# Performance work log

Hardware: AMD Instinct MI355X
Metric: run time of the kernel (lower is better)

The kernel has to match this reference:

```python
import jax, jax.numpy as jnp
import numpy as np

N, K, E = 100000, 256, 3200000
IN_C, H1, H2 = 5, 16, 32


def _glorot(key, shape):
    fan = shape[0]
    return jax.random.normal(key, shape, jnp.float32) / np.float32(np.sqrt(fan))


def setup_inputs() -> dict:
    key = jax.random.key(0)
    ks = jax.random.split(key, 14)
    x = jax.random.normal(ks[0], (N, IN_C), jnp.float32)
    edge_index = jax.random.randint(ks[1], (2, E), 0, N, dtype=jnp.int64)
    edge_attr = jax.random.uniform(ks[2], (E,), jnp.float32)
    pos = jax.random.uniform(ks[3], (N, K), jnp.float32)  # soft cluster assignment s_c
    return {
        "x": x, "edge_index": edge_index, "edge_attr": edge_attr, "pos": pos,
        # SplineConv1 (kernel_size=1 -> single kernel weight + root + bias)
        "W1": _glorot(ks[4], (IN_C, H1)), "root1": _glorot(ks[5], (IN_C, H1)),
        "b1": jnp.zeros((H1,), jnp.float32),
        # SplineConv2
        "W2": _glorot(ks[6], (H1, H2)), "root2": _glorot(ks[7], (H1, H2)),
        "b2": jnp.zeros((H2,), jnp.float32),
        # MLP head
        "lw1": _glorot(ks[8], (H2, 8)), "lb1": jnp.zeros((8,), jnp.float32),
        "lw2": _glorot(ks[9], (8, 2)), "lb2": jnp.zeros((2,), jnp.float32),
    }


def _leaky(v):
    return jnp.where(v > 0, v, 0.1 * v)


def reference(x, edge_index, edge_attr, pos, W1, root1, b1, W2, root2, b2, lw1, lb1, lw2, lb2):
    n = x.shape[0]
    src, dst = edge_index[0], edge_index[1]  # source_to_target flow

    # --- SplineConv(5,16,dim=1,kernel_size=1): mean_j (x_j @ W) + x @ root + b ---
    msg = x[src] @ W1                                      # [E,16]
    agg = jax.ops.segment_sum(msg, dst, num_segments=n)    # [N,16]
    deg = jax.ops.segment_sum(jnp.ones((msg.shape[0],), x.dtype), dst, num_segments=n)
    h = agg / jnp.maximum(deg, 1.0)[:, None] + x @ root1 + b1
    h = _leaky(jax.nn.relu(h))                             # relu then LeakyReLU(0.1)

    # --- pooling: x' = s_c^T h ; adj = s_c^T A s_c (A sparse with edge_attr values) ---
    xp = pos.T @ h                                          # [K,16]
    A_sc = jax.ops.segment_sum(edge_attr[:, None] * pos[dst], src, num_segments=n)  # spmm: [N,K]
    adj = pos.T @ A_sc                                      # [K,K]

    # --- nonzero/coalesce -> edge list of adj; SplineConv(16,32) on pooled graph ---
    # kernel_size=1 => edge values irrelevant; only the nonzero pattern (connectivity) matters.
    mask = (adj != 0).astype(x.dtype)                       # [K,K], row=src, col=dst
    xw = xp @ W2                                            # [K,32]
    deg2 = mask.sum(axis=0)                                 # in-degree per target
    agg2 = (mask.T @ xw) / jnp.maximum(deg2, 1.0)[:, None]
    h2 = agg2 + xp @ root2 + b2
    h2 = _leaky(jax.nn.relu(h2))                            # [K,32]

    # --- global mean pool (single graph) + MLP head, return x[0] ---
    g = h2.mean(axis=0)                                     # [32]
    out = _leaky(g @ lw1 + lb1) @ lw2 + lb2                 # [2]
    return out
```

## Files before the change

### kernel.cpp

```cpp
#include <hip/hip_runtime.h>

#define INC 5
#define H1C 16
#define H2C 32
#define KCL 256

#define NBINS 40
#define BINSZ 2500
#define MAXCHUNK 12

#define PB_SHIFT 9
#define PB_SZ 512
#define PB_NBMAX 256
#define PB_C 18432
#define PB_M 6144
#define PB_ETPB 6
#define PB_S 2
#define PB_GMAX 9216
#define PB_GETG 9

#define POOL_NB 512
#define PT 32

typedef __attribute__((address_space(1))) const unsigned gls_src;
typedef __attribute__((address_space(3))) unsigned gls_dst;

__global__ void k_setup(const float* __restrict__ x, float* __restrict__ x8,
                        const unsigned int* __restrict__ ei, int* __restrict__ flag,
                        unsigned* __restrict__ gcur, int N, int NB) {
    int n = blockIdx.x * blockDim.x + threadIdx.x;
    if (n < N) {
        const float* xr = x + (size_t)n * INC;
        float4* o = (float4*)(x8 + (size_t)n * 8);
        o[0] = make_float4(xr[0], xr[1], xr[2], xr[3]);
        o[1] = make_float4(xr[4], 0.0f, 0.0f, 0.0f);
    }
    if (blockIdx.x == 0) {
        if (threadIdx.x < (unsigned)NB) gcur[threadIdx.x] = (unsigned)threadIdx.x * PB_C;
        if (threadIdx.x == 0) {
            int is64 = 1;
            for (int i = 1; i < 32; i += 2)
                if (ei[i] != 0u) is64 = 0;
            *flag = is64;
        }
    }
}

__global__ void k_detect(const unsigned int* __restrict__ ei, int* __restrict__ flag) {
    if (blockIdx.x == 0 && threadIdx.x == 0) {
        int is64 = 1;
        for (int i = 1; i < 32; i += 2)
            if (ei[i] != 0u) is64 = 0;
        *flag = is64;
    }
}

__global__ __launch_bounds__(1024) void k_part(const unsigned int* __restrict__ ei,
                                               const int* __restrict__ flag,
                                               unsigned* __restrict__ gcur,
                                               unsigned* __restrict__ bucket,
                                               int E, int NB) {
    __shared__ int hist[PB_NBMAX];
    __shared__ int lbase[PB_NBMAX];
    __shared__ unsigned gbase[PB_NBMAX];
    __shared__ int sc[PB_NBMAX];
    __shared__ unsigned sorted[PB_M];
    __shared__ unsigned char sbin[PB_M];

    const int tid = threadIdx.x;
    const int e0 = blockIdx.x * PB_M;
    int m = E - e0; if (m > PB_M) m = PB_M;

    for (int i = tid; i < PB_NBMAX; i += 1024) hist[i] = 0;
    __syncthreads();

    const int is64 = *flag;
    unsigned ee[PB_ETPB]; int eb[PB_ETPB]; int er[PB_ETPB];

#pragma unroll
    for (int ii = 0; ii < PB_ETPB; ii++) {
        const int off = tid + ii * 1024;
        eb[ii] = -1; ee[ii] = 0u; er[ii] = 0;
        if (off < m) {
            const int e = e0 + off;
            unsigned d, s;
            if (is64) { d = ei[2 * ((size_t)E + (size_t)e)]; s = ei[2 * (size_t)e]; }
            else      { d = ei[(size_t)E + (size_t)e];       s = ei[(size_t)e]; }
            const int b = (int)(d >> PB_SHIFT);
            eb[ii] = b;
            ee[ii] = (s << PB_SHIFT) | (d & (PB_SZ - 1));
            er[ii] = atomicAdd(&hist[b], 1);
        }
    }
    __syncthreads();

    if (tid < PB_NBMAX) sc[tid] = hist[tid];
    __syncthreads();
    for (int st = 1; st < PB_NBMAX; st <<= 1) {
        int v = 0;
        if (tid < PB_NBMAX && tid >= st) v = sc[tid - st];
        __syncthreads();
        if (tid < PB_NBMAX) sc[tid] += v;
        __syncthreads();
    }
    if (tid < PB_NBMAX) lbase[tid] = sc[tid] - hist[tid];
    if (tid < NB) gbase[tid] = atomicAdd(&gcur[tid], (unsigned)hist[tid]);
    __syncthreads();

#pragma unroll
    for (int ii = 0; ii < PB_ETPB; ii++) {
        if (eb[ii] >= 0) {
            const int j = lbase[eb[ii]] + er[ii];
            sorted[j] = ee[ii];
            sbin[j] = (unsigned char)eb[ii];
        }
    }
    __syncthreads();

    for (int j = tid; j < m; j += 1024) {
        const int b = (int)sbin[j];
        const unsigned g = gbase[b] + (unsigned)(j - lbase[b]);
        if (g < (unsigned)(b + 1) * PB_C) bucket[g] = sorted[j];
    }
}

__global__ __launch_bounds__(1024) void k_gather(const unsigned* __restrict__ bucket,
                                                 const unsigned* __restrict__ gcur,
                                                 const float* __restrict__ x8,
                                                 float* __restrict__ part,
                                                 int N, int NB) {
    __shared__ unsigned sorted[PB_GMAX];
    __shared__ int hist[PB_SZ];
    __shared__ int sc[PB_SZ];
    __shared__ int lbase[PB_SZ];
    __shared__ float stage[PB_SZ * 6];

    const int b = blockIdx.x / PB_S;
    const int sub = blockIdx.x % PB_S;
    const int tid = threadIdx.x;
    const int lo = b << PB_SHIFT;
    int hi = lo + PB_SZ; if (hi > N) hi = N;
    const int nloc = hi - lo;

    int cnt = (int)(gcur[b] - (unsigned)b * PB_C);
    if (cnt > PB_C) cnt = PB_C;
    const int i0 = (cnt * sub) / PB_S;
    const int i1 = (cnt * (sub + 1)) / PB_S;
    const int m = i1 - i0;
    const unsigned* bk = bucket + (size_t)b * PB_C + i0;

    for (int i = tid; i < PB_SZ; i += 1024) hist[i] = 0;
    __syncthreads();

    unsigned ee[PB_GETG]; int edl[PB_GETG]; int er[PB_GETG];
#pragma unroll
    for (int ii = 0; ii < PB_GETG; ii++) {
        const int off = tid + ii * 1024;
        edl[ii] = -1; ee[ii] = 0u; er[ii] = 0;
        if (off < m) {
            const unsigned e = bk[off];
            const int dl = (int)(e & (PB_SZ - 1));
            edl[ii] = dl;
            ee[ii] = e;
            er[ii] = atomicAdd(&hist[dl], 1);
        }
    }
    __syncthreads();

    if (tid < PB_SZ) sc[tid] = hist[tid];
    __syncthreads();
    for (int st = 1; st < PB_SZ; st <<= 1) {
        int v = 0;
        if (tid < PB_SZ && tid >= st) v = sc[tid - st];
        __syncthreads();
        if (tid < PB_SZ) sc[tid] += v;
        __syncthreads();
    }
    if (tid < PB_SZ) lbase[tid] = sc[tid] - hist[tid];
    __syncthreads();

#pragma unroll
    for (int ii = 0; ii < PB_GETG; ii++)
        if (edl[ii] >= 0) sorted[lbase[edl[ii]] + er[ii]] = ee[ii];
    __syncthreads();

    const int node = tid & (PB_SZ - 1);
    const int half = tid >> PB_SHIFT;
    const int start = lbase[node];
    const int len = hist[node];
    const int js = start + (half ? (len >> 1) : 0);
    const int je = start + (half ? len : (len >> 1));
    float a0 = 0.f, a1 = 0.f, a2 = 0.f, a3 = 0.f, a4 = 0.f;
    for (int j = js; j < je; j++) {
        const unsigned s = sorted[j] >> PB_SHIFT;
        const float4 xr4 = *(const float4*)(x8 + (size_t)s * 8);
        const float xr5 = x8[(size_t)s * 8 + 4];
        a0 += xr4.x; a1 += xr4.y; a2 += xr4.z; a3 += xr4.w; a4 += xr5;
    }
    if (half) {
        float* st = stage + node * 6;
        st[0] = a0; st[1] = a1; st[2] = a2; st[3] = a3; st[4] = a4;
    }
    __syncthreads();
    if (!half && node < nloc) {
        const float* st = stage + node * 6;
        float* o = part + (size_t)sub * ((size_t)N * 6) + (size_t)(lo + node) * 6;
        o[0] = a0 + st[0];
        o[1] = a1 + st[1];
        o[2] = a2 + st[2];
        o[3] = a3 + st[3];
        o[4] = a4 + st[4];
        o[5] = (float)len;
    }
}

__global__ __launch_bounds__(1024) void k_edge_bin(const unsigned int* __restrict__ ei,
                                                   const float* __restrict__ x,
                                                   const int* __restrict__ flag,
                                                   float* __restrict__ part,
                                                   int E, int nchunk, int N) {
    __shared__ float acc[BINSZ * 6];
    const int bin = blockIdx.x % NBINS;
    const int chunk = blockIdx.x / NBINS;
    const int lo = bin * BINSZ;
    const int hi = (lo + BINSZ < N) ? (lo + BINSZ) : N;
    const int nloc = hi - lo;
    for (int i = threadIdx.x; i < nloc * 6; i += 1024) acc[i] = 0.0f;
    __syncthreads();

    const int is64 = *flag;
    const long long ce = ((long long)E + nchunk - 1) / nchunk;
    const long long e0 = (long long)chunk * ce;
    long long e1 = e0 + ce;
    if (e1 > E) e1 = E;

    for (long long e = e0 + threadIdx.x; e < e1; e += 1024) {
        const int d = is64 ? (int)ei[2 * ((size_t)E + (size_t)e)] : (int)ei[(size_t)E + (size_t)e];
        if (d >= lo && d < hi) {
            const int s = is64 ? (int)ei[2 * (size_t)e] : (int)ei[(size_t)e];
            const float* xr = x + (size_t)s * INC;
            float* a = acc + (d - lo) * 6;
            atomicAdd(a + 0, xr[0]);
            atomicAdd(a + 1, xr[1]);
            atomicAdd(a + 2, xr[2]);
            atomicAdd(a + 3, xr[3]);
            atomicAdd(a + 4, xr[4]);
            atomicAdd(a + 5, 1.0f);
        }
    }
    __syncthreads();
    float* o = part + (size_t)chunk * ((size_t)N * 6) + (size_t)lo * 6;
    for (int i = threadIdx.x; i < nloc * 6; i += 1024) o[i] = acc[i];
}

__global__ void k_node2(const float* __restrict__ x, const float* __restrict__ part,
                        const float* __restrict__ W1, const float* __restrict__ root1,
                        const float* __restrict__ b1, float* __restrict__ h,
                        int N, int nchunk) {
    int n = blockIdx.x * blockDim.x + threadIdx.x;
    if (n >= N) return;
    float s[6] = {0.f, 0.f, 0.f, 0.f, 0.f, 0.f};
    for (int c = 0; c < nchunk; c++) {
        const float* p = part + (size_t)c * ((size_t)N * 6) + (size_t)n * 6;
#pragma unroll
        for (int j = 0; j < 6; j++) s[j] += p[j];
    }
    const float inv = 1.0f / fmaxf(s[5], 1.0f);
    float xs[INC], xv[INC];
#pragma unroll
    for (int c = 0; c < INC; c++) {
        xs[c] = s[c] * inv;
        xv[c] = x[(size_t)n * INC + c];
    }
    float hv[H1C];
#pragma unroll
    for (int j = 0; j < H1C; j++) {
        float v = b1[j];
#pragma unroll
        for (int c = 0; c < INC; c++)
            v = fmaf(xs[c], W1[c * H1C + j], fmaf(xv[c], root1[c * H1C + j], v));
        hv[j] = fmaxf(v, 0.0f);
    }
    float4* hp = (float4*)(h + (size_t)n * H1C);
#pragma unroll
    for (int q = 0; q < 4; q++)
        hp[q] = make_float4(hv[4 * q], hv[4 * q + 1], hv[4 * q + 2], hv[4 * q + 3]);
}

__global__ __launch_bounds__(512) void k_pool(const float* __restrict__ pos,
                                              const float* __restrict__ h,
                                              float* __restrict__ xp_part, int N, int nb) {
    __shared__ float pbuf[2][PT * KCL];
    __shared__ float hbuf[2][PT * H1C];
    const int tid = threadIdx.x;
    const int k = tid & 255;
    const int jh = tid >> 8;
    const int wid = tid >> 6;
    const int lane = tid & 63;
    const int chunk = (N + nb - 1) / nb;
    const int n0 = blockIdx.x * chunk;
    const int n1 = min(n0 + chunk, N);
    const int ntile = (n1 > n0) ? (n1 - n0 + PT - 1) / PT : 0;

    const size_t maxp = (size_t)N * KCL - 4;
    const size_t maxh = (size_t)N * H1C - 4;

    float acc[8];
#pragma unroll
    for (int j = 0; j < 8; j++) acc[j] = 0.0f;

    auto STAGE = [&](int bf, int tile) {
        const size_t nt0 = (size_t)n0 + (size_t)tile * PT;
        const size_t pb = nt0 * KCL;
#pragma unroll
        for (int c = 0; c < 4; ++c) {
            const int off = (wid * 4 + c) * 256;
            size_t fi = pb + (size_t)off + (size_t)lane * 4;
            if (fi > maxp) fi = maxp;
            __builtin_amdgcn_global_load_lds((gls_src*)(pos + fi),
                                             (gls_dst*)&pbuf[bf][off], 16, 0, 0);
        }
        if (wid < 2) {
            const int off = wid * 256;
            size_t fi = nt0 * H1C + (size_t)off + (size_t)lane * 4;
            if (fi > maxh) fi = maxh;
            __builtin_amdgcn_global_load_lds((gls_src*)(h + fi),
                                             (gls_dst*)&hbuf[bf][off], 16, 0, 0);
        }
    };

    int buf = 0;
    if (ntile > 0) {
        STAGE(0, 0);
        __syncthreads();
    }
    for (int t = 0; t < ntile; ++t) {
        if (t + 1 < ntile) STAGE(buf ^ 1, t + 1);
        const int nt0 = n0 + t * PT;
        const int tcnt = min(PT, n1 - nt0);
        for (int tt = 0; tt < tcnt; ++tt) {
            const float p = pbuf[buf][tt * KCL + k];
            const float4* hr = (const float4*)&hbuf[buf][tt * H1C + jh * 8];
            const float4 ha = hr[0], hb = hr[1];
            acc[0] = fmaf(p, ha.x, acc[0]); acc[1] = fmaf(p, ha.y, acc[1]);
            acc[2] = fmaf(p, ha.z, acc[2]); acc[3] = fmaf(p, ha.w, acc[3]);
            acc[4] = fmaf(p, hb.x, acc[4]); acc[5] = fmaf(p, hb.y, acc[5]);
            acc[6] = fmaf(p, hb.z, acc[6]); acc[7] = fmaf(p, hb.w, acc[7]);
        }
        __syncthreads();
        buf ^= 1;
    }

    float* o = xp_part + (size_t)blockIdx.x * (KCL * H1C) + k * H1C + jh * 8;
    *(float4*)o = make_float4(acc[0], acc[1], acc[2], acc[3]);
    *(float4*)(o + 4) = make_float4(acc[4], acc[5], acc[6], acc[7]);
}

__global__ __launch_bounds__(1024) void k_xpred(const float* __restrict__ xp_part,
                                                float* __restrict__ xp, int nb) {
    __shared__ float r[1024];
    const int li = threadIdx.x & 63;
    const int sub = threadIdx.x >> 6;
    const int i = blockIdx.x * 64 + li;
    float s = 0.0f;
    for (int b = sub; b < nb; b += 16) s += xp_part[(size_t)b * (KCL * H1C) + i];
    r[threadIdx.x] = s;
    __syncthreads();
    if (threadIdx.x < 512) r[threadIdx.x] += r[threadIdx.x + 512];
    __syncthreads();
    if (threadIdx.x < 256) r[threadIdx.x] += r[threadIdx.x + 256];
    __syncthreads();
    if (threadIdx.x < 128) r[threadIdx.x] += r[threadIdx.x + 128];
    __syncthreads();
    if (threadIdx.x < 64) xp[i] = r[threadIdx.x] + r[threadIdx.x + 64];
}

__global__ __launch_bounds__(256) void k_tail(const float* __restrict__ xp,
                                              const float* __restrict__ W2,
                                              const float* __restrict__ root2,
                                              const float* __restrict__ b2,
                                              const float* __restrict__ lw1,
                                              const float* __restrict__ lb1,
                                              const float* __restrict__ lw2,
                                              const float* __restrict__ lb2,
                                              float* __restrict__ out) {
    __shared__ float red[4][H2C];
    __shared__ float bcast[H2C];
    const int t = threadIdx.x;
    const int wv = t >> 6;
    const int lane = t & 63;

    float row[H1C];
#pragma unroll
    for (int c = 0; c < H1C; c++) row[c] = xp[t * H1C + c];

    float v1[H2C];
#pragma unroll
    for (int j = 0; j < H2C; j++) {
        float v = 0.0f;
#pragma unroll
        for (int c = 0; c < H1C; c++) v = fmaf(row[c], W2[c * H2C + j], v);
        v1[j] = v;
    }
#pragma unroll
    for (int off = 1; off < 64; off <<= 1) {
#pragma unroll
        for (int j = 0; j < H2C; j++) v1[j] += __shfl_xor(v1[j], off);
    }
    if (lane == 0) {
#pragma unroll
        for (int j = 0; j < H2C; j++) red[wv][j] = v1[j];
    }
    __syncthreads();
    if (t < H2C) bcast[t] = red[0][t] + red[1][t] + red[2][t] + red[3][t];
    __syncthreads();

    float v2[H2C];
#pragma unroll
    for (int j = 0; j < H2C; j++) {
        float v = bcast[j] * (1.0f / KCL) + b2[j];
#pragma unroll
        for (int c = 0; c < H1C; c++) v = fmaf(row[c], root2[c * H2C + j], v);
        v2[j] = fmaxf(v, 0.0f);
    }
#pragma unroll
    for (int off = 1; off < 64; off <<= 1) {
#pragma unroll
        for (int j = 0; j < H2C; j++) v2[j] += __shfl_xor(v2[j], off);
    }
    if (lane == 0) {
#pragma unroll
        for (int j = 0; j < H2C; j++) red[wv][j] = v2[j];
    }
    __syncthreads();

    if (t == 0) {
        float g[H2C];
#pragma unroll
        for (int j = 0; j < H2C; j++)
            g[j] = (red[0][j] + red[1][j] + red[2][j] + red[3][j]) * (1.0f / KCL);
        float u[8];
#pragma unroll
        for (int a = 0; a < 8; a++) {
            float v = lb1[a];
#pragma unroll
            for (int j = 0; j < H2C; j++) v = fmaf(g[j], lw1[j * 8 + a], v);
            u[a] = v > 0.0f ? v : 0.1f * v;
        }
#pragma unroll
        for (int o = 0; o < 2; o++) {
            float v = lb2[o];
#pragma unroll
            for (int a = 0; a < 8; a++) v = fmaf(u[a], lw2[a * 2 + o], v);
            out[o] = v;
        }
    }
}

extern "C" void kernel_launch(void* const* d_in, const int* in_sizes, int n_in,
                              void* d_out, int out_size, void* d_ws, size_t ws_size,
                              hipStream_t stream) {
    const float* x         = (const float*)d_in[0];
    const unsigned int* ei = (const unsigned int*)d_in[1];
    const float* pos   = (const float*)d_in[3];
    const float* W1    = (const float*)d_in[4];
    const float* root1 = (const float*)d_in[5];
    const float* b1    = (const float*)d_in[6];
    const float* W2    = (const float*)d_in[7];
    const float* root2 = (const float*)d_in[8];
    const float* b2    = (const float*)d_in[9];
    const float* lw1   = (const float*)d_in[10];
    const float* lb1   = (const float*)d_in[11];
    const float* lw2   = (const float*)d_in[12];
    const float* lb2   = (const float*)d_in[13];
    float* out = (float*)d_out;

    const int N = in_sizes[0] / INC;
    const int E = in_sizes[1] / 2;
    const int NB = (N + PB_SZ - 1) >> PB_SHIFT;

    float* ws    = (float*)d_ws;
    float* xp    = ws;
    int*   flag  = (int*)(xp + KCL * H1C);
    float* h     = (float*)(flag + 16);
    float* regio = h + (size_t)N * H1C;

    const size_t pref_floats = (size_t)(KCL * H1C) + 16 + (size_t)N * H1C;
    const size_t region_floats = ws_size / 4 > pref_floats ? ws_size / 4 - pref_floats : 0;
    const size_t fast_floats = (size_t)PB_S * N * 6 + (size_t)N * 8 + (size_t)NB * PB_C + 256;

    if (region_floats >= fast_floats && N <= 131072 && NB <= PB_NBMAX) {
        float* part      = regio;
        float* x8        = part + (size_t)PB_S * N * 6;
        unsigned* bucket = (unsigned*)(x8 + (size_t)N * 8);
        unsigned* gcur   = bucket + (size_t)NB * PB_C;
        const int P = (E + PB_M - 1) / PB_M;

        k_setup<<<(N + 255) / 256, 256, 0, stream>>>(x, x8, ei, flag, gcur, N, NB);
        k_part<<<P, 1024, 0, stream>>>(ei, flag, gcur, bucket, E, NB);
        k_gather<<<NB * PB_S, 1024, 0, stream>>>(bucket, gcur, x8, part, N, NB);
        k_node2<<<(N + 255) / 256, 256, 0, stream>>>(x, part, W1, root1, b1, h, N, PB_S);

        float* xp_part = x8;
        k_pool<<<POOL_NB, 512, 0, stream>>>(pos, h, xp_part, N, POOL_NB);
        k_xpred<<<64, 1024, 0, stream>>>(xp_part, xp, POOL_NB);
    } else {
        size_t avail = region_floats > (size_t)POOL_NB * KCL * H1C
                     ? region_floats - (size_t)POOL_NB * KCL * H1C : 0;
        int nchunk = (int)(avail / ((size_t)N * 6));
        if (nchunk > MAXCHUNK) nchunk = MAXCHUNK;
        if (nchunk < 1) nchunk = 1;
        float* part = regio;
        float* xp_part = part + (size_t)nchunk * N * 6;
        k_detect<<<1, 64, 0, stream>>>(ei, flag);
        k_edge_bin<<<NBINS * nchunk, 1024, 0, stream>>>(ei, x, flag, part, E, nchunk, N);
        k_node2<<<(N + 255) / 256, 256, 0, stream>>>(x, part, W1, root1, b1, h, N, nchunk);
        k_pool<<<POOL_NB, 512, 0, stream>>>(pos, h, xp_part, N, POOL_NB);
        k_xpred<<<64, 1024, 0, stream>>>(xp_part, xp, POOL_NB);
    }
    k_tail<<<1, 256, 0, stream>>>(xp, W2, root2, b2, lw1, lb1, lw2, lb2, out);
}
```

Before: 118.0 us.

## Register-block pool kernel over 4 clusters per thread with node-split reduction

Restructures k_pool so each thread accumulates a 4x8 register tile (4 clusters by 8 hidden channels) using float4 LDS reads of pos, with the node loop split across four wave groups. The per-group partial sums are then combined through shared memory in a two-step tree before the write-out. The goal is fewer LDS loads per FMA in the inner loop. The cost is more registers, an added reduction phase with extra syncs, and a launch-bounds occupancy hint of 2 blocks per CU.

```diff
diff --git a/kernel.cpp b/kernel.cpp
--- a/kernel.cpp
+++ b/kernel.cpp
@@ -287,16 +287,16 @@
         hp[q] = make_float4(hv[4 * q], hv[4 * q + 1], hv[4 * q + 2], hv[4 * q + 3]);
 }
 
-__global__ __launch_bounds__(512) void k_pool(const float* __restrict__ pos,
-                                              const float* __restrict__ h,
-                                              float* __restrict__ xp_part, int N, int nb) {
+__global__ __launch_bounds__(512, 2) void k_pool(const float* __restrict__ pos,
+                                                 const float* __restrict__ h,
+                                                 float* __restrict__ xp_part, int N, int nb) {
     __shared__ float pbuf[2][PT * KCL];
     __shared__ float hbuf[2][PT * H1C];
     const int tid = threadIdx.x;
-    const int k = tid & 255;
-    const int jh = tid >> 8;
+    const int lane = tid & 63;
     const int wid = tid >> 6;
-    const int lane = tid & 63;
+    const int jh = wid & 1;
+    const int ns = wid >> 1;
     const int chunk = (N + nb - 1) / nb;
     const int n0 = blockIdx.x * chunk;
     const int n1 = min(n0 + chunk, N);
@@ -305,9 +305,11 @@
     const size_t maxp = (size_t)N * KCL - 4;
     const size_t maxh = (size_t)N * H1C - 4;
 
-    float acc[8];
-#pragma unroll
-    for (int j = 0; j < 8; j++) acc[j] = 0.0f;
+    float acc[4][8];
+#pragma unroll
+    for (int c = 0; c < 4; c++)
+#pragma unroll
+        for (int d = 0; d < 8; d++) acc[c][d] = 0.0f;
 
     auto STAGE = [&](int bf, int tile) {
         const size_t nt0 = (size_t)n0 + (size_t)tile * PT;
@@ -338,22 +340,67 @@
         if (t + 1 < ntile) STAGE(buf ^ 1, t + 1);
         const int nt0 = n0 + t * PT;
         const int tcnt = min(PT, n1 - nt0);
-        for (int tt = 0; tt < tcnt; ++tt) {
-            const float p = pbuf[buf][tt * KCL + k];
-            const float4* hr = (const float4*)&hbuf[buf][tt * H1C + jh * 8];
-            const float4 ha = hr[0], hb = hr[1];
-            acc[0] = fmaf(p, ha.x, acc[0]); acc[1] = fmaf(p, ha.y, acc[1]);
-            acc[2] = fmaf(p, ha.z, acc[2]); acc[3] = fmaf(p, ha.w, acc[3]);
-            acc[4] = fmaf(p, hb.x, acc[4]); acc[5] = fmaf(p, hb.y, acc[5]);
-            acc[6] = fmaf(p, hb.z, acc[6]); acc[7] = fmaf(p, hb.w, acc[7]);
+#pragma unroll 2
+        for (int tt = ns; tt < tcnt; tt += 4) {
+            const float4 p = *(const float4*)&pbuf[buf][tt * KCL + 4 * lane];
+            const float4 hA = *(const float4*)&hbuf[buf][tt * H1C + jh * 8];
+            const float4 hB = *(const float4*)&hbuf[buf][tt * H1C + jh * 8 + 4];
+            const float pk[4] = {p.x, p.y, p.z, p.w};
+            const float hv[8] = {hA.x, hA.y, hA.z, hA.w, hB.x, hB.y, hB.z, hB.w};
+#pragma unroll
+            for (int c = 0; c < 4; c++)
+#pragma unroll
+                for (int d = 0; d < 8; d++)
+                    acc[c][d] = fmaf(pk[c], hv[d], acc[c][d]);
         }
         __syncthreads();
         buf ^= 1;
     }
 
-    float* o = xp_part + (size_t)blockIdx.x * (KCL * H1C) + k * H1C + jh * 8;
-    *(float4*)o = make_float4(acc[0], acc[1], acc[2], acc[3]);
-    *(float4*)(o + 4) = make_float4(acc[4], acc[5], acc[6], acc[7]);
+    float* sred = &pbuf[0][0];
+    if (ns == 1 || ns == 3) {
+        float* sl = sred + ((ns - 1) >> 1) * 4096 + jh * 2048 + lane;
+#pragma unroll
+        for (int c = 0; c < 4; c++)
+#pragma unroll
+            for (int d = 0; d < 8; d++) sl[(c * 8 + d) * 64] = acc[c][d];
+    }
+    __syncthreads();
+    if (ns == 0 || ns == 2) {
+        const float* sl = sred + (ns >> 1) * 4096 + jh * 2048 + lane;
+#pragma unroll
+        for (int c = 0; c < 4; c++)
+#pragma unroll
+            for (int d = 0; d < 8; d++) acc[c][d] += sl[(c * 8 + d) * 64];
+    }
+    __syncthreads();
+    if (ns == 2) {
+        float* sl = sred + jh * 2048 + lane;
+#pragma unroll
+        for (int c = 0; c < 4; c++)
+#pragma unroll
+            for (int d = 0; d < 8; d++) sl[(c * 8 + d) * 64] = acc[c][d];
+    }
+    __syncthreads();
+    if (ns == 0) {
+        const float* sl = sred + jh * 2048 + lane;
+        float* o = xp_part + (size_t)blockIdx.x * (KCL * H1C);
+#pragma unroll
+        for (int c = 0; c < 4; c++) {
+            float4 r0, r1;
+            r0.x = acc[c][0] + sl[(c * 8 + 0) * 64];
+            r0.y = acc[c][1] + sl[(c * 8 + 1) * 64];
+            r0.z = acc[c][2] + sl[(c * 8 + 2) * 64];
+            r0.w = acc[c][3] + sl[(c * 8 + 3) * 64];
+            r1.x = acc[c][4] + sl[(c * 8 + 4) * 64];
+            r1.y = acc[c][5] + sl[(c * 8 + 5) * 64];
+            r1.z = acc[c][6] + sl[(c * 8 + 6) * 64];
+            r1.w = acc[c][7] + sl[(c * 8 + 7) * 64];
+            float* oc = o + (4 * lane + c) * H1C + jh * 8;
+            *(float4*)oc = r0;
+            *(float4*)(oc + 4) = r1;
+        }
+    }
 }
 
 __global__ __launch_bounds__(1024) void k_xpred(const float* __restrict__ xp_part,
```

Result: faster. 110.5 us (-6.3%).
